# Kernel optimization log

Measured on AMD Instinct MI355X. Metric: run time of the kernel, lower is better.

The kernel has to match this reference:

```python
import jax, jax.numpy as jnp
import numpy as np

B, T, H, FUT = 256, 512, 128, 512


def setup_inputs() -> dict:
    key = jax.random.key(0)
    ks = jax.random.split(key, 24)
    s = 1.0 / np.sqrt(H)

    def u(k, shape, scale):
        return jax.random.uniform(k, shape, jnp.float32, -scale, scale)

    inp = {
        "input": jax.random.normal(ks[0], (B, T), jnp.float32),
        "future": FUT,
        # LSTMCell 1 (input size 1)
        "Wih1": u(ks[1], (4 * H, 1), s), "Whh1": u(ks[2], (4 * H, H), s),
        "bih1": u(ks[3], (4 * H,), s), "bhh1": u(ks[4], (4 * H,), s),
        # LSTMCell 2
        "Wih2": u(ks[5], (4 * H, H), s), "Whh2": u(ks[6], (4 * H, H), s),
        "bih2": u(ks[7], (4 * H,), s), "bhh2": u(ks[8], (4 * H,), s),
        # LSTMCell 3
        "Wih3": u(ks[9], (4 * H, H), s), "Whh3": u(ks[10], (4 * H, H), s),
        "bih3": u(ks[11], (4 * H,), s), "bhh3": u(ks[12], (4 * H,), s),
        # MultiheadAttention packed in-proj (q,k,v) and out-proj
        "in_proj_w": u(ks[13], (3 * H, H), s), "in_proj_b": u(ks[14], (3 * H,), s),
        "out_w": u(ks[15], (H, H), s), "out_b": u(ks[16], (H,), s),
        # final Linear(H, 1)
        "lin_w": u(ks[17], (1, H), s), "lin_b": u(ks[18], (1,), s),
    }
    return inp


def _lstm_cell(x, h, c, Wih, Whh, bih, bhh):
    # torch LSTMCell gate order: i, f, g, o
    g = x @ Wih.T + h @ Whh.T + (bih + bhh)
    i, f, gg, o = jnp.split(g, 4, axis=-1)
    c_new = jax.nn.sigmoid(f) * c + jax.nn.sigmoid(i) * jnp.tanh(gg)
    h_new = jax.nn.sigmoid(o) * jnp.tanh(c_new)
    return h_new, c_new


def _forward(input, Wih1, Whh1, bih1, bhh1, Wih2, Whh2, bih2, bhh2,
             Wih3, Whh3, bih3, bhh3, in_proj_w, in_proj_b, out_w, out_b,
             lin_w, lin_b, future):
    hd = in_proj_w.shape[1]
    # seq_len == 1 attention: softmax over a single key is 1, so
    # attn_output = out_proj(v_proj(h3)); q/k play no role in the output.
    Wv = in_proj_w[2 * hd:]
    bv = in_proj_b[2 * hd:]

    def head(h3):
        attn = (h3 @ Wv.T + bv) @ out_w.T + out_b
        return attn @ lin_w.T + lin_b  # [B, 1]

    def step(states, x_t):
        h1, c1, h2, c2, h3, c3 = states
        h1, c1 = _lstm_cell(x_t, h1, c1, Wih1, Whh1, bih1, bhh1)
        h2, c2 = _lstm_cell(h1, h2, c2, Wih2, Whh2, bih2, bhh2)
        h3, c3 = _lstm_cell(h2, h3, c3, Wih3, Whh3, bih3, bhh3)
        return (h1, c1, h2, c2, h3, c3), head(h3)

    n = input.shape[0]
    z = jnp.zeros((n, hd), input.dtype)
    init = (z, z, z, z, z, z)

    xs = input.T[:, :, None]  # [T, B, 1]
    states, outs = jax.lax.scan(lambda s, x: step(s, x), init, xs)

    def fstep(carry, _):
        st, out = carry
        st, out = step(st, out)
        return (st, out), out

    (_, _), fouts = jax.lax.scan(fstep, (states, outs[-1]), None, length=future)
    all_outs = jnp.concatenate([outs, fouts], axis=0)  # [T+future, B, 1]
    return all_outs[..., 0].T  # [B, T+future]


def reference(input, Wih1, Whh1, bih1, bhh1, Wih2, Whh2, bih2, bhh2,
              Wih3, Whh3, bih3, bhh3, in_proj_w, in_proj_b, out_w, out_b,
              lin_w, lin_b, future):
    return _forward(input, Wih1, Whh1, bih1, bhh1, Wih2, Whh2, bih2, bhh2,
                    Wih3, Whh3, bih3, bhh3, in_proj_w, in_proj_b, out_w,
                    out_b, lin_w, lin_b, future)
```

## Files before the change

### kernel.cpp

```cpp
#include <hip/hip_runtime.h>


typedef _Float16 f16;
typedef _Float16 f16x2 __attribute__((ext_vector_type(2)));
typedef unsigned int u32;

#define T_IN 512
#define T_TOT 1024
#define NBLK 128

__device__ __forceinline__ f16x2 u2h(u32 u) { return __builtin_bit_cast(f16x2, u); }

__device__ __forceinline__ float fdot2f(f16x2 a, f16x2 b, float c) {
#if __has_builtin(__builtin_amdgcn_fdot2)
  return __builtin_amdgcn_fdot2(a, b, c, false);
#else
  return c + (float)a[0] * (float)b[0] + (float)a[1] * (float)b[1];
#endif
}

__device__ __forceinline__ float frcp(float x) {
#if __has_builtin(__builtin_amdgcn_rcpf)
  return __builtin_amdgcn_rcpf(x);
#else
  return 1.f / x;
#endif
}
__device__ __forceinline__ float fsigm(float x) { return frcp(1.f + __expf(-x)); }
__device__ __forceinline__ float ftanh(float x) { return 1.f - 2.f * frcp(1.f + __expf(2.f * x)); }

#define DOT4(acc, w, hv)                     \
  do {                                       \
    f16x2 _h = u2h(hv);                      \
    acc[0] = fdot2f(u2h((w).x), _h, acc[0]); \
    acc[1] = fdot2f(u2h((w).y), _h, acc[1]); \
    acc[2] = fdot2f(u2h((w).z), _h, acc[2]); \
    acc[3] = fdot2f(u2h((w).w), _h, acc[3]); \
  } while (0)

__global__ void pack_stream(u32* dst, const float* Wih2, const float* Whh2,
                            const float* Wih3, const float* Whh3) {
  int tid = blockIdx.x * 256 + threadIdx.x;
  if (tid >= 64 * 512 * 4) return;
  int g = tid & 3;
  int t = (tid >> 2) & 511;
  int s = tid >> 11;
  int idx = t >> 2, kq = t & 3;
  const float* src;
  int p;
  if (s < 48) {
    int q = s / 6, rmd = s % 6;
    if (rmd < 4) {
      p = kq * 32 + 4 * q + rmd;
      if (p < 64) { src = Wih2; } else { src = Whh2; p -= 64; }
    } else {
      p = kq * 16 + 2 * q + (rmd - 4);
      src = Whh3;
    }
  } else {
    p = kq * 16 + (s - 48);
    src = Wih3;
  }
  int j = g * 128 + idx;
  union { f16 h[2]; u32 u; } cv;
  cv.h[0] = (f16)src[j * 128 + 2 * p];
  cv.h[1] = (f16)src[j * 128 + 2 * p + 1];
  dst[tid] = cv.u;
}

__global__ void pack1s(u32* dst, const float* Whh1) {
  int tid = blockIdx.x * 256 + threadIdx.x;
  if (tid >= 16 * 512 * 4) return;
  int g = tid & 3;
  int t = (tid >> 2) & 511;
  int q = tid >> 11;
  int idx = t >> 2, kq = t & 3;
  int p = kq * 16 + q;
  int j = g * 128 + idx;
  union { f16 h[2]; u32 u; } cv;
  cv.h[0] = (f16)Whh1[j * 128 + 2 * p];
  cv.h[1] = (f16)Whh1[j * 128 + 2 * p + 1];
  dst[tid] = cv.u;
}

__global__ void prep_cons(float* cons, const float* a1, const float* b1,
                          const float* a2, const float* b2,
                          const float* a3, const float* b3, const float* wih1) {
  int tid = blockIdx.x * 256 + threadIdx.x;
  if (tid >= 2048) return;
  int gg = tid >> 9, g = (tid >> 7) & 3, idx = tid & 127;
  int j = g * 128 + idx;
  float v;
  if (gg == 0) v = a1[j] + b1[j];
  else if (gg == 1) v = a2[j] + b2[j];
  else if (gg == 2) v = a3[j] + b3[j];
  else v = wih1[j];
  cons[tid] = v;
}

__global__ void head_fold(float* cons, const float* lin_w, const float* out_w,
                          const float* Wv, const float* bv,
                          const float* out_b, const float* lin_b) {
  __shared__ float wlo[128];
  __shared__ float pr[128];
  int j = threadIdx.x;
  float s = 0.f;
  for (int k = 0; k < 128; ++k) s += lin_w[k] * out_w[k * 128 + j];
  wlo[j] = s;
  __syncthreads();
  float t = 0.f;
  for (int k = 0; k < 128; ++k) t += wlo[k] * Wv[k * 128 + j];
  cons[2048 + j] = t;
  pr[j] = s * bv[j] + lin_w[j] * out_b[j];
  __syncthreads();
  if (j == 0) {
    float b = lin_b[0];
    for (int k = 0; k < 128; ++k) b += pr[k];
    cons[2176] = b;
  }
}

__global__ __launch_bounds__(512)
__attribute__((amdgpu_waves_per_eu(2))) void pendulum_persist(
    const float* __restrict__ input, const uint4* __restrict__ WT1s,
    const uint4* __restrict__ WS, const float* __restrict__ consG,
    float* __restrict__ out) {
  __shared__ __align__(16) uint4 w1s[8192];
  __shared__ __align__(16) f16 h1b[2][2][128];
  __shared__ __align__(16) f16 h2b[2][2][128];
  __shared__ __align__(16) f16 h3b[2][128];
  __shared__ float xin[2][T_IN];
  __shared__ float consL[2180];
  __shared__ float redp[2][8];

  const int t = threadIdx.x;
  const int idx = t >> 2;
  const int kq = t & 3;
  const int row0 = blockIdx.x * 2, row1 = row0 + 1;

  for (int e = t; e < 8192; e += 512) w1s[e] = WT1s[e];
  for (int e = t; e < 2177; e += 512) consL[e] = consG[e];
  for (int e = t; e < 1024; e += 512)
    xin[e >> 9][e & 511] = input[(row0 + (e >> 9)) * T_IN + (e & 511)];
  if (t < 128) {
    h1b[0][0][t] = (f16)0.f; h1b[0][1][t] = (f16)0.f;
    h1b[1][0][t] = (f16)0.f; h1b[1][1][t] = (f16)0.f;
    h2b[0][0][t] = (f16)0.f; h2b[0][1][t] = (f16)0.f;
    h2b[1][0][t] = (f16)0.f; h2b[1][1][t] = (f16)0.f;
    h3b[0][t] = (f16)0.f;    h3b[1][t] = (f16)0.f;
  }

  const uint4* Wp = WS + t;
  const uint4* w1p = w1s + t;

  float c1a = 0.f, c1b = 0.f, c2a = 0.f, c2b = 0.f, c3a = 0.f, c3b = 0.f;
  float y0 = 0.f, y1 = 0.f;
  __syncthreads();
  const float beffv = consL[2176];

  {
    float x0 = xin[0][0], x1 = xin[1][0];
    if (kq == 0) {
      float b0 = consL[idx], b2v = consL[256 + idx], b3v = consL[384 + idx];
      float w0 = consL[1536 + idx], w2w = consL[1792 + idx],
            w3w = consL[1920 + idx];
      {
        float ig = fsigm(b0 + x0 * w0);
        float gg = ftanh(b2v + x0 * w2w), og = fsigm(b3v + x0 * w3w);
        c1a = ig * gg; h1b[0][0][idx] = (f16)(og * ftanh(c1a));
      }
      {
        float ig = fsigm(b0 + x1 * w0);
        float gg = ftanh(b2v + x1 * w2w), og = fsigm(b3v + x1 * w3w);
        c1b = ig * gg; h1b[0][1][idx] = (f16)(og * ftanh(c1b));
      }
    }
    __syncthreads();
  }

  uint4 ring[8];
#pragma unroll
  for (int c = 0; c < 8; ++c) ring[c] = Wp[c * 512];

  for (int s = 0; s < T_TOT; ++s) {
    const int par = s & 1;
    const int xi = (s + 1 < T_IN) ? (s + 1) : 0;
    float xl0 = xin[0][xi];
    float xl1 = xin[1][xi];

    const uint4* hL2r0 = (kq < 2)
        ? (const uint4*)&h1b[par][0][0] + kq * 8
        : (const uint4*)&h2b[par ^ 1][0][0] + (kq - 2) * 8;
    const uint4* hL2r1 = (kq < 2)
        ? (const uint4*)&h1b[par][1][0] + kq * 8
        : (const uint4*)&h2b[par ^ 1][1][0] + (kq - 2) * 8;
    const uint4* h3r0 = (const uint4*)&h3b[0][0] + kq * 4;
    const uint4* h3r1 = (const uint4*)&h3b[1][0] + kq * 4;

    float a2r0[4] = {0, 0, 0, 0}, a2r1[4] = {0, 0, 0, 0};
    float a3r0[4] = {0, 0, 0, 0}, a3r1[4] = {0, 0, 0, 0};

    uint4 E0, E1;
#pragma unroll
    for (int q = 0; q < 8; ++q) {
      uint4 H0 = hL2r0[q], H1 = hL2r1[q];
      u32 e0[4] = {H0.x, H0.y, H0.z, H0.w};
      u32 e1[4] = {H1.x, H1.y, H1.z, H1.w};
      if ((q & 1) == 0) { E0 = h3r0[q >> 1]; E1 = h3r1[q >> 1]; }
#pragma unroll
      for (int m = 0; m < 4; ++m) {
        const int sl = 6 * q + m;
        uint4 w = ring[sl & 7];
        ring[sl & 7] = Wp[((sl + 8) & 63) * 512];
        DOT4(a2r0, w, e0[m]);
        DOT4(a2r1, w, e1[m]);
      }
      {
        const int sl = 6 * q + 4;
        uint4 w = ring[sl & 7];
        ring[sl & 7] = Wp[((sl + 8) & 63) * 512];
        u32 h0 = (q & 1) ? E0.z : E0.x, h1v = (q & 1) ? E1.z : E1.x;
        DOT4(a3r0, w, h0);
        DOT4(a3r1, w, h1v);
      }
      {
        const int sl = 6 * q + 5;
        uint4 w = ring[sl & 7];
        ring[sl & 7] = Wp[((sl + 8) & 63) * 512];
        u32 h0 = (q & 1) ? E0.w : E0.y, h1v = (q & 1) ? E1.w : E1.y;
        DOT4(a3r0, w, h0);
        DOT4(a3r1, w, h1v);
      }
    }

#pragma unroll
    for (int g = 0; g < 4; ++g) {
      a2r0[g] += __shfl_xor(a2r0[g], 1, 64); a2r0[g] += __shfl_xor(a2r0[g], 2, 64);
      a2r1[g] += __shfl_xor(a2r1[g], 1, 64); a2r1[g] += __shfl_xor(a2r1[g], 2, 64);
    }
    if (kq == 0) {
      float b0 = consL[512 + idx], b1v = consL[640 + idx],
            b2v = consL[768 + idx], b3v = consL[896 + idx];
      {
        float ig = fsigm(a2r0[0] + b0), fg = fsigm(a2r0[1] + b1v);
        float gg = ftanh(a2r0[2] + b2v), og = fsigm(a2r0[3] + b3v);
        c2a = fg * c2a + ig * gg;
        h2b[par][0][idx] = (f16)(og * ftanh(c2a));
      }
      {
        float ig = fsigm(a2r1[0] + b0), fg = fsigm(a2r1[1] + b1v);
        float gg = ftanh(a2r1[2] + b2v), og = fsigm(a2r1[3] + b3v);
        c2b = fg * c2b + ig * gg;
        h2b[par][1][idx] = (f16)(og * ftanh(c2b));
      }
    }
    asm volatile("s_waitcnt lgkmcnt(0)\n\ts_barrier" ::: "memory");

    const uint4* hLTr0 = (const uint4*)&h2b[par][0][0] + kq * 4;
    const uint4* hLTr1 = (const uint4*)&h2b[par][1][0] + kq * 4;
    const uint4* h1r0 = (const uint4*)&h1b[par][0][0] + kq * 4;
    const uint4* h1r1 = (const uint4*)&h1b[par][1][0] + kq * 4;

    float a1r0[4] = {0, 0, 0, 0}, a1r1[4] = {0, 0, 0, 0};
    uint4 L0, L1v, F0, F1;
#pragma unroll
    for (int q = 0; q < 8; ++q) {
      if ((q & 1) == 0) {
        L0 = hLTr0[q >> 1]; L1v = hLTr1[q >> 1];
        F0 = h1r0[q >> 1];  F1 = h1r1[q >> 1];
      }
      {
        const int sl = 48 + 2 * q;
        uint4 w = ring[sl & 7];
        ring[sl & 7] = Wp[((sl + 8) & 63) * 512];
        u32 h0 = (q & 1) ? L0.z : L0.x, h1x = (q & 1) ? L1v.z : L1v.x;
        DOT4(a3r0, w, h0);
        DOT4(a3r1, w, h1x);
      }
      {
        const int sl = 48 + 2 * q + 1;
        uint4 w = ring[sl & 7];
        ring[sl & 7] = Wp[((sl + 8) & 63) * 512];
        u32 h0 = (q & 1) ? L0.w : L0.y, h1x = (q & 1) ? L1v.w : L1v.y;
        DOT4(a3r0, w, h0);
        DOT4(a3r1, w, h1x);
      }
      {
        uint4 w = w1p[(2 * q) * 512];
        u32 h0 = (q & 1) ? F0.z : F0.x, h1x = (q & 1) ? F1.z : F1.x;
        DOT4(a1r0, w, h0);
        DOT4(a1r1, w, h1x);
      }
      {
        uint4 w = w1p[(2 * q + 1) * 512];
        u32 h0 = (q & 1) ? F0.w : F0.y, h1x = (q & 1) ? F1.w : F1.y;
        DOT4(a1r0, w, h0);
        DOT4(a1r1, w, h1x);
      }
    }

#pragma unroll
    for (int g = 0; g < 4; ++g) {
      a3r0[g] += __shfl_xor(a3r0[g], 1, 64); a3r0[g] += __shfl_xor(a3r0[g], 2, 64);
      a3r1[g] += __shfl_xor(a3r1[g], 1, 64); a3r1[g] += __shfl_xor(a3r1[g], 2, 64);
      a1r0[g] += __shfl_xor(a1r0[g], 1, 64); a1r0[g] += __shfl_xor(a1r0[g], 2, 64);
      a1r1[g] += __shfl_xor(a1r1[g], 1, 64); a1r1[g] += __shfl_xor(a1r1[g], 2, 64);
    }

    float p0 = 0.f, p1 = 0.f;
    if (kq == 0) {
      float b0 = consL[1024 + idx], b1v = consL[1152 + idx],
            b2v = consL[1280 + idx], b3v = consL[1408 + idx];
      float weffr = consL[2048 + idx];
      {
        float ig = fsigm(a3r0[0] + b0), fg = fsigm(a3r0[1] + b1v);
        float gg = ftanh(a3r0[2] + b2v), og = fsigm(a3r0[3] + b3v);
        c3a = fg * c3a + ig * gg;
        float h3 = og * ftanh(c3a);
        h3b[0][idx] = (f16)h3;
        p0 = weffr * h3;
      }
      {
        float ig = fsigm(a3r1[0] + b0), fg = fsigm(a3r1[1] + b1v);
        float gg = ftanh(a3r1[2] + b2v), og = fsigm(a3r1[3] + b3v);
        c3b = fg * c3b + ig * gg;
        float h3 = og * ftanh(c3b);
        h3b[1][idx] = (f16)h3;
        p1 = weffr * h3;
      }
    }
#pragma unroll
    for (int k = 1; k < 64; k <<= 1) {
      p0 += __shfl_xor(p0, k, 64);
      p1 += __shfl_xor(p1, k, 64);
    }
    if ((t & 63) == 0) { redp[0][t >> 6] = p0; redp[1][t >> 6] = p1; }
    asm volatile("s_waitcnt lgkmcnt(0)\n\ts_barrier" ::: "memory");

    y0 = beffv; y1 = beffv;
#pragma unroll
    for (int w8 = 0; w8 < 8; ++w8) { y0 += redp[0][w8]; y1 += redp[1][w8]; }
    if (t == 0) out[row0 * T_TOT + s] = y0;
    else if (t == 1) out[row1 * T_TOT + s] = y1;

    float xv0 = (s + 1 < T_IN) ? xl0 : y0;
    float xv1 = (s + 1 < T_IN) ? xl1 : y1;
    if (kq == 0) {
      float b0 = consL[idx], b1v = consL[128 + idx], b2v = consL[256 + idx],
            b3v = consL[384 + idx];
      float w0 = consL[1536 + idx], w1w = consL[1664 + idx],
            w2w = consL[1792 + idx], w3w = consL[1920 + idx];
      {
        float ig = fsigm(a1r0[0] + b0 + xv0 * w0), fg = fsigm(a1r0[1] + b1v + xv0 * w1w);
        float gg = ftanh(a1r0[2] + b2v + xv0 * w2w), og = fsigm(a1r0[3] + b3v + xv0 * w3w);
        c1a = fg * c1a + ig * gg;
        h1b[par ^ 1][0][idx] = (f16)(og * ftanh(c1a));
      }
      {
        float ig = fsigm(a1r1[0] + b0 + xv1 * w0), fg = fsigm(a1r1[1] + b1v + xv1 * w1w);
        float gg = ftanh(a1r1[2] + b2v + xv1 * w2w), og = fsigm(a1r1[3] + b3v + xv1 * w3w);
        c1b = fg * c1b + ig * gg;
        h1b[par ^ 1][1][idx] = (f16)(og * ftanh(c1b));
      }
    }
    asm volatile("s_waitcnt lgkmcnt(0)\n\ts_barrier" ::: "memory");
  }
}

extern "C" void kernel_launch(void* const* d_in, const int* in_sizes, int n_in,
                              void* d_out, int out_size, void* d_ws, size_t ws_size,
                              hipStream_t stream) {
  const float* input = (const float*)d_in[0];
  const float* Wih1 = (const float*)d_in[2];
  const float* Whh1 = (const float*)d_in[3];
  const float* bih1 = (const float*)d_in[4];
  const float* bhh1 = (const float*)d_in[5];
  const float* Wih2 = (const float*)d_in[6];
  const float* Whh2 = (const float*)d_in[7];
  const float* bih2 = (const float*)d_in[8];
  const float* bhh2 = (const float*)d_in[9];
  const float* Wih3 = (const float*)d_in[10];
  const float* Whh3 = (const float*)d_in[11];
  const float* bih3 = (const float*)d_in[12];
  const float* bhh3 = (const float*)d_in[13];
  const float* in_proj_w = (const float*)d_in[14];
  const float* in_proj_b = (const float*)d_in[15];
  const float* out_w = (const float*)d_in[16];
  const float* out_b = (const float*)d_in[17];
  const float* lin_w = (const float*)d_in[18];
  const float* lin_b = (const float*)d_in[19];

  char* ws = (char*)d_ws;
  u32* WT1s = (u32*)(ws + (0 << 10));
  u32* WS = (u32*)(ws + (128 << 10));
  float* consG = (float*)(ws + (640 << 10));

  pack1s<<<128, 256, 0, stream>>>(WT1s, Whh1);
  pack_stream<<<512, 256, 0, stream>>>(WS, Wih2, Whh2, Wih3, Whh3);
  prep_cons<<<8, 256, 0, stream>>>(consG, bih1, bhh1, bih2, bhh2, bih3, bhh3, Wih1);
  head_fold<<<1, 128, 0, stream>>>(consG, lin_w, out_w,
                                   in_proj_w + 2 * 128 * 128, in_proj_b + 256,
                                   out_b, lin_b);

  pendulum_persist<<<NBLK, 512, 0, stream>>>(
      input, (const uint4*)WT1s, (const uint4*)WS, consG, (float*)d_out);
}
```

Baseline: 9.260 ms.

## Pin layer-3 LSTM weights in AGPR registers instead of streaming from global

Splits the weight packing so layer-3 weights (Wih3, Whh3) are packed separately and loaded once per thread into 128 accumulation registers at kernel start. The per-step weight stream from global memory then covers only layer-2 weights (32 slots instead of 64), which halves the per-timestep memory traffic. The cost is a v_accvgpr_read per weight word inside the loop and higher register pressure, which could cause spills or limit occupancy at 512 threads.

Measured after the change: 12.30 ms. 32.9% more time.

```diff
diff --git a/kernel.cpp b/kernel.cpp
--- a/kernel.cpp
+++ b/kernel.cpp
@@ -38,33 +38,38 @@
     acc[3] = fdot2f(u2h((w).w), _h, acc[3]); \
   } while (0)
 
-__global__ void pack_stream(u32* dst, const float* Wih2, const float* Whh2,
-                            const float* Wih3, const float* Whh3) {
+__global__ void pack_stream(u32* dst, const float* Wih2, const float* Whh2) {
   int tid = blockIdx.x * 256 + threadIdx.x;
-  if (tid >= 64 * 512 * 4) return;
+  if (tid >= 32 * 512 * 4) return;
   int g = tid & 3;
   int t = (tid >> 2) & 511;
   int s = tid >> 11;
   int idx = t >> 2, kq = t & 3;
+  int p = kq * 32 + s;
   const float* src;
-  int p;
-  if (s < 48) {
-    int q = s / 6, rmd = s % 6;
-    if (rmd < 4) {
-      p = kq * 32 + 4 * q + rmd;
-      if (p < 64) { src = Wih2; } else { src = Whh2; p -= 64; }
-    } else {
-      p = kq * 16 + 2 * q + (rmd - 4);
-      src = Whh3;
-    }
-  } else {
-    p = kq * 16 + (s - 48);
-    src = Wih3;
-  }
+  if (p < 64) { src = Wih2; } else { src = Whh2; p -= 64; }
   int j = g * 128 + idx;
   union { f16 h[2]; u32 u; } cv;
   cv.h[0] = (f16)src[j * 128 + 2 * p];
   cv.h[1] = (f16)src[j * 128 + 2 * p + 1];
+  dst[tid] = cv.u;
+}
+
+__global__ void pack3r(u32* dst, const float* Wih3, const float* Whh3) {
+  int tid = blockIdx.x * 256 + threadIdx.x;
+  if (tid >= 32 * 512 * 4) return;
+  int g = tid & 3;
+  int t = (tid >> 2) & 511;
+  int slot = tid >> 11;
+  int idx = t >> 2, kq = t & 3;
+  const float* src;
+  int cp;
+  if (slot < 16) { src = Whh3; cp = kq * 16 + slot; }
+  else           { src = Wih3; cp = kq * 16 + (slot - 16); }
+  int j = g * 128 + idx;
+  union { f16 h[2]; u32 u; } cv;
+  cv.h[0] = (f16)src[j * 128 + 2 * cp];
+  cv.h[1] = (f16)src[j * 128 + 2 * cp + 1];
   dst[tid] = cv.u;
 }
 
@@ -120,11 +125,22 @@
   }
 }
 
+#define AGW(i, v) \
+  asm volatile("v_accvgpr_write_b32 %0, %1" : "=a"(ag[i]) : "v"(v))
+#define AGR4(slot, w4)                                            \
+  asm volatile("v_accvgpr_read_b32 %0, %4\n\t"                    \
+               "v_accvgpr_read_b32 %1, %5\n\t"                    \
+               "v_accvgpr_read_b32 %2, %6\n\t"                    \
+               "v_accvgpr_read_b32 %3, %7"                        \
+               : "=v"((w4).x), "=v"((w4).y), "=v"((w4).z), "=v"((w4).w) \
+               : "a"(ag[4 * (slot) + 0]), "a"(ag[4 * (slot) + 1]),      \
+                 "a"(ag[4 * (slot) + 2]), "a"(ag[4 * (slot) + 3]))
+
 __global__ __launch_bounds__(512)
 __attribute__((amdgpu_waves_per_eu(2))) void pendulum_persist(
     const float* __restrict__ input, const uint4* __restrict__ WT1s,
-    const uint4* __restrict__ WS, const float* __restrict__ consG,
-    float* __restrict__ out) {
+    const uint4* __restrict__ WS, const uint4* __restrict__ WR,
+    const float* __restrict__ consG, float* __restrict__ out) {
   __shared__ __align__(16) uint4 w1s[8192];
   __shared__ __align__(16) f16 h1b[2][2][128];
   __shared__ __align__(16) f16 h2b[2][2][128];
@@ -150,6 +166,16 @@
     h3b[0][t] = (f16)0.f;    h3b[1][t] = (f16)0.f;
   }
 
+  u32 ag[128];
+#pragma unroll
+  for (int sl2 = 0; sl2 < 32; ++sl2) {
+    uint4 v = WR[sl2 * 512 + t];
+    AGW(4 * sl2 + 0, v.x);
+    AGW(4 * sl2 + 1, v.y);
+    AGW(4 * sl2 + 2, v.z);
+    AGW(4 * sl2 + 3, v.w);
+  }
+
   const uint4* Wp = WS + t;
   const uint4* w1p = w1s + t;
 
@@ -209,24 +235,22 @@
       if ((q & 1) == 0) { E0 = h3r0[q >> 1]; E1 = h3r1[q >> 1]; }
 #pragma unroll
       for (int m = 0; m < 4; ++m) {
-        const int sl = 6 * q + m;
+        const int sl = 4 * q + m;
         uint4 w = ring[sl & 7];
-        ring[sl & 7] = Wp[((sl + 8) & 63) * 512];
+        ring[sl & 7] = Wp[((sl + 8) & 31) * 512];
         DOT4(a2r0, w, e0[m]);
         DOT4(a2r1, w, e1[m]);
       }
       {
-        const int sl = 6 * q + 4;
-        uint4 w = ring[sl & 7];
-        ring[sl & 7] = Wp[((sl + 8) & 63) * 512];
+        uint4 w;
+        AGR4(2 * q, w);
         u32 h0 = (q & 1) ? E0.z : E0.x, h1v = (q & 1) ? E1.z : E1.x;
         DOT4(a3r0, w, h0);
         DOT4(a3r1, w, h1v);
       }
       {
-        const int sl = 6 * q + 5;
-        uint4 w = ring[sl & 7];
-        ring[sl & 7] = Wp[((sl + 8) & 63) * 512];
+        uint4 w;
+        AGR4(2 * q + 1, w);
         u32 h0 = (q & 1) ? E0.w : E0.y, h1v = (q & 1) ? E1.w : E1.y;
         DOT4(a3r0, w, h0);
         DOT4(a3r1, w, h1v);
@@ -270,17 +294,15 @@
         F0 = h1r0[q >> 1];  F1 = h1r1[q >> 1];
       }
       {
-        const int sl = 48 + 2 * q;
-        uint4 w = ring[sl & 7];
-        ring[sl & 7] = Wp[((sl + 8) & 63) * 512];
+        uint4 w;
+        AGR4(16 + 2 * q, w);
         u32 h0 = (q & 1) ? L0.z : L0.x, h1x = (q & 1) ? L1v.z : L1v.x;
         DOT4(a3r0, w, h0);
         DOT4(a3r1, w, h1x);
       }
       {
-        const int sl = 48 + 2 * q + 1;
-        uint4 w = ring[sl & 7];
-        ring[sl & 7] = Wp[((sl + 8) & 63) * 512];
+        uint4 w;
+        AGR4(16 + 2 * q + 1, w);
         u32 h0 = (q & 1) ? L0.w : L0.y, h1x = (q & 1) ? L1v.w : L1v.y;
         DOT4(a3r0, w, h0);
         DOT4(a3r1, w, h1x);
@@ -393,15 +415,18 @@
   char* ws = (char*)d_ws;
   u32* WT1s = (u32*)(ws + (0 << 10));
   u32* WS = (u32*)(ws + (128 << 10));
+  u32* WR = (u32*)(ws + (384 << 10));
   float* consG = (float*)(ws + (640 << 10));
 
   pack1s<<<128, 256, 0, stream>>>(WT1s, Whh1);
-  pack_stream<<<512, 256, 0, stream>>>(WS, Wih2, Whh2, Wih3, Whh3);
+  pack_stream<<<256, 256, 0, stream>>>(WS, Wih2, Whh2);
+  pack3r<<<256, 256, 0, stream>>>(WR, Wih3, Whh3);
   prep_cons<<<8, 256, 0, stream>>>(consG, bih1, bhh1, bih2, bhh2, bih3, bhh3, Wih1);
   head_fold<<<1, 128, 0, stream>>>(consG, lin_w, out_w,
                                    in_proj_w + 2 * 128 * 128, in_proj_b + 256,
                                    out_b, lin_b);
 
   pendulum_persist<<<NBLK, 512, 0, stream>>>(
-      input, (const uint4*)WT1s, (const uint4*)WS, consG, (float*)d_out);
-}
+      input, (const uint4*)WT1s, (const uint4*)WS, (const uint4*)WR,
+      consG, (float*)d_out);
+}
```
